# Kernel optimization log

Measured on AMD Instinct MI355X. Metric: run time of the kernel, lower is better.

The kernel has to match this reference:

```python
import jax, jax.numpy as jnp
import numpy as np

NQ = 12          # num_qubits
NL = 5           # num_layers
NA = 4           # num_actions
DIM = 2 ** NQ    # state-vector dimension

# PennyLane convention: wire 0 is the most-significant bit of the state index.
_idx = np.arange(DIM)
_bits = (_idx[:, None] >> (NQ - 1 - np.arange(NQ))) & 1           # [DIM, NQ]
_cz = np.ones(DIM)
for _i in range(NQ):                                              # ring of CZs (all diagonal -> fuse)
    _cz *= np.where((_bits[:, _i] & _bits[:, (_i + 1) % NQ]) == 1, -1.0, 1.0)
CZ_RING = jnp.asarray(_cz, dtype=jnp.complex64)                   # [DIM]
ZTAB = jnp.asarray(1 - 2 * _bits[:, :NA], dtype=jnp.float32)      # [DIM, NA] PauliZ eigenvalues


def _bc(v):
    # broadcast an angle-derived scalar or [B] vector against [B, lead, trail]
    v = jnp.asarray(v)
    return v.reshape(v.shape + (1, 1))


def _apply_1q(state, wire, m00, m01, m10, m11):
    b = state.shape[0]
    lead, trail = 2 ** wire, 2 ** (NQ - 1 - wire)
    s = state.reshape(b, lead, 2, trail)
    s0, s1 = s[:, :, 0, :], s[:, :, 1, :]
    return jnp.stack([m00 * s0 + m01 * s1, m10 * s0 + m11 * s1], axis=2).reshape(b, DIM)


def _rx(state, wire, theta):
    c = _bc(jnp.cos(0.5 * theta)).astype(jnp.complex64)
    s = _bc(jnp.sin(0.5 * theta)).astype(jnp.complex64)
    return _apply_1q(state, wire, c, -1j * s, -1j * s, c)


def _ry(state, wire, theta):
    c = _bc(jnp.cos(0.5 * theta)).astype(jnp.complex64)
    s = _bc(jnp.sin(0.5 * theta)).astype(jnp.complex64)
    return _apply_1q(state, wire, c, -s, s, c)


def _rz(state, wire, theta):
    # diagonal gate: no mixing across the wire axis
    b = state.shape[0]
    lead, trail = 2 ** wire, 2 ** (NQ - 1 - wire)
    e = _bc(jnp.exp(-0.5j * theta))  # e^{-i t/2}; conj(e) = e^{+i t/2} for real t
    s = state.reshape(b, lead, 2, trail)
    return jnp.stack([e * s[:, :, 0, :], jnp.conj(e) * s[:, :, 1, :]], axis=2).reshape(b, DIM)


def setup_inputs() -> dict:
    key = jax.random.key(0)
    k1, k2 = jax.random.split(key)
    x = jax.random.normal(k1, (4096, 4 * NQ), dtype=jnp.float32)
    input_scaling = jnp.ones((NL, 3, NQ), dtype=jnp.float32)
    weights = jax.random.uniform(k2, (NL, 3, 2 * NQ), dtype=jnp.float32,
                                 minval=-np.pi, maxval=np.pi)
    output_scaling = jnp.ones((NA,), dtype=jnp.float32)
    return {"x": x, "input_scaling": input_scaling, "weights": weights,
            "output_scaling": output_scaling}


def reference(x, input_scaling, weights, output_scaling):
    b = x.shape[0]
    feats = (x[:, NQ:2 * NQ], x[:, 2 * NQ:3 * NQ], x[:, 3 * NQ:4 * NQ])
    state = jnp.zeros((b, DIM), dtype=jnp.complex64).at[:, 0].set(1.0)
    for layer in range(NL):
        for blk in range(3):
            f = feats[blk]
            for i in range(NQ):
                state = _rx(state, i, input_scaling[layer, blk, i] * f[:, i])
            for i in range(NQ):
                state = _ry(state, i, weights[layer, blk, i])
            for i in range(NQ):
                state = _rz(state, i, weights[layer, blk, i + NQ])
            state = state * CZ_RING[None, :]
    probs = state.real ** 2 + state.imag ** 2          # [B, DIM]
    expvals = probs @ ZTAB                             # [B, NA] <Z_i>
    return expvals * output_scaling                    # logits
```

## Files before the change

kernel.cpp:

```cpp
#include <hip/hip_runtime.h>
#include <stdint.h>

#define NQ 12
#define NL 5
#define NIT 15
#define AMPS 16


typedef float f2 __attribute__((ext_vector_type(2)));

static __device__ __forceinline__ float f_u(unsigned u) { return __uint_as_float(u); }
static __device__ __forceinline__ unsigned u_f(float f) { return __float_as_uint(f); }

#define PK_MUL_RR(acc, C, S) \
    asm("v_pk_mul_f32 %0, %1, %2 op_sel_hi:[0,1]" : "=v"(acc) : "v"(C), "v"(S))
#define PK_FMA_I(acc, C, S) \
    asm("v_pk_fma_f32 %0, %1, %2, %0 op_sel:[1,1,0] op_sel_hi:[1,0,1] neg_lo:[1,0,0]" \
        : "+v"(acc) : "v"(C), "v"(S))
#define PK_FMA_R(acc, C, S) \
    asm("v_pk_fma_f32 %0, %1, %2, %0 op_sel_hi:[0,1,1]" : "+v"(acc) : "v"(C), "v"(S))
#define PK_FMA_IC(acc, C, S) \
    asm("v_pk_fma_f32 %0, %1, %2, %0 op_sel:[1,1,0] op_sel_hi:[1,0,1] neg_hi:[1,0,0]" \
        : "+v"(acc) : "v"(C), "v"(S))
#define PK_FMA_RN(acc, C, S) \
    asm("v_pk_fma_f32 %0, %1, %2, %0 op_sel_hi:[0,1,1] neg_lo:[1,0,0] neg_hi:[1,0,0]" \
        : "+v"(acc) : "v"(C), "v"(S))

#define CMUL(DST, CA, CB) \
    { PK_MUL_RR(DST, CA, CB); PK_FMA_I(DST, CA, CB); }

#define CPLX_AB(DST, CA, S, CB, O)                                    \
    { f2 t_;                                                          \
      PK_MUL_RR(t_, CA, S); PK_FMA_I(t_, CA, S);                      \
      PK_FMA_R (t_, CB, O); PK_FMA_I(t_, CB, O);                      \
      DST = t_; }

template <int CTRL>
static __device__ __forceinline__ float dpp_xor(float v) {
    int u = (int)__float_as_uint(v);
    return __uint_as_float((unsigned)__builtin_amdgcn_update_dpp(u, u, CTRL, 0xF, 0xF, false));
}
static __device__ __forceinline__ float swz_xor4(float v) {
    return f_u((unsigned)__builtin_amdgcn_ds_swizzle((int)u_f(v), 0x101F));
}

#define AB_GATE_PK(OPX)                                                 \
    _Pragma("unroll")                                                   \
    for (int r = 0; r < AMPS; ++r) {                                    \
        f2 o; o.x = OPX(s[r].x); o.y = OPX(s[r].y);                     \
        CPLX_AB(s[r], CA, s[r], CB, o)                                  \
    }

template <int ST>
static __device__ __forceinline__ void reg_gate_pk(f2 (&s)[AMPS], f2 CAg, f2 CBg) {
#pragma unroll
    for (int r0 = 0; r0 < AMPS; ++r0) {
        if (r0 & ST) continue;
        const int r1 = r0 | ST;
        const f2 s0 = s[r0], s1 = s[r1];
        f2 t0, t1;
        PK_MUL_RR(t0, CAg, s0); PK_FMA_I (t0, CAg, s0);
        PK_FMA_R (t0, CBg, s1); PK_FMA_I (t0, CBg, s1);
        PK_MUL_RR(t1, CAg, s1); PK_FMA_IC(t1, CAg, s1);
        PK_FMA_RN(t1, CBg, s0); PK_FMA_I (t1, CBg, s0);
        s[r0] = t0; s[r1] = t1;
    }
}

__global__ __launch_bounds__(256)
void qsim_kernel(
    const float* __restrict__ x,
    const float* __restrict__ iscale,
    const float* __restrict__ w,
    const float* __restrict__ oscale,
    float* __restrict__ out,
    int batch)
{
    const int tid  = threadIdx.x;
    const int lane = tid & 63;
    const int wv   = tid >> 6;
    const int b    = blockIdx.x;

    __shared__ float4 xch[8 * 256];
    __shared__ float4 coef[NIT * NQ];

    if (tid < NIT * NQ) {
        const int it  = tid / NQ;
        const int q   = tid - it * NQ;
        const int blk = it - 3 * (it / 3);
        const float* xb = x + (size_t)b * (4 * NQ);
        float f     = xb[NQ + blk * NQ + q];
        float alpha = iscale[it * NQ + q] * f;
        float beta  = w[it * 2 * NQ + q];
        float gamma = w[it * 2 * NQ + NQ + q];
        float sa, ca, sb, cb, sg, cg;
        sincosf(0.5f * alpha, &sa, &ca);
        sincosf(0.5f * beta,  &sb, &cb);
        sincosf(0.5f * gamma, &sg, &cg);
        float cbca = cb * ca, sbsa = sb * sa, sbca = sb * ca, cbsa = cb * sa;
        float ar =  cg * cbca + sg * sbsa;
        float ai =  cg * sbsa - sg * cbca;
        float br = -(cg * sbca + sg * cbsa);
        float bi =  sg * sbca - cg * cbsa;
        coef[tid] = make_float4(ar, ai, br, bi);
    }

    f2 s[AMPS];
#pragma unroll
    for (int r = 0; r < AMPS; ++r) { s[r].x = 0.f; s[r].y = 0.f; }
    if (tid == 0) s[0].x = 1.f;

    unsigned czm = 0;
#pragma unroll
    for (int r = 0; r < AMPS; ++r) {
        unsigned idx  = ((unsigned)wv << 10) | ((unsigned)lane << 4) | (unsigned)r;
        unsigned adj  = (idx & (idx >> 1)) & 0x7FFu;
        unsigned wrap = (idx & (idx >> 11)) & 1u;
        czm |= (((unsigned)__popc(adj) + wrap) & 1u) << r;
    }

    const unsigned sw1 = (unsigned)((wv >> 1) & 1) << 31;
    const unsigned sw0 = (unsigned)(wv & 1) << 31;
    const bool hb2 = (lane >> 5) & 1;
    const bool hb3 = (lane >> 4) & 1;
    const unsigned sb4 = (unsigned)((lane >> 3) & 1) << 31;
    const unsigned sb5 = (unsigned)((lane >> 2) & 1) << 31;
    const unsigned sb6 = (unsigned)((lane >> 1) & 1) << 31;
    const unsigned sb7 = (unsigned)(lane & 1) << 31;

    const int t64  = tid ^ 64;
    const int t128 = tid ^ 128;
    const int t192 = tid ^ 192;

    __syncthreads();

#pragma unroll 1
    for (int it = 0; it < NIT; ++it) {
        float4 c[NQ];
#pragma unroll
        for (int q = 0; q < NQ; ++q) c[q] = coef[it * NQ + q];

        {
            const f2 A0 = { c[0].x, f_u(u_f(c[0].y) ^ sw1) };
            const f2 B0 = { f_u(u_f(c[0].z) ^ sw1), c[0].w };
            const f2 A1 = { c[1].x, f_u(u_f(c[1].y) ^ sw0) };
            const f2 B1 = { f_u(u_f(c[1].z) ^ sw0), c[1].w };
            f2 Cs, C64, C128, C192;
            CMUL(Cs,   A0, A1)
            CMUL(C64,  A0, B1)
            CMUL(C128, B0, A1)
            CMUL(C192, B0, B1)

            __syncthreads();
#pragma unroll
            for (int k = 0; k < 8; ++k)
                xch[(k << 8) + tid] = make_float4(s[2*k].x, s[2*k].y, s[2*k+1].x, s[2*k+1].y);
            __syncthreads();
#pragma unroll
            for (int k = 0; k < 8; ++k) {
                const float4 p1 = xch[(k << 8) + t64];
                const float4 p2 = xch[(k << 8) + t128];
                const float4 p3 = xch[(k << 8) + t192];
                {
                    const f2 o1 = { p1.x, p1.y }, o2 = { p2.x, p2.y }, o3 = { p3.x, p3.y };
                    f2 t0;
                    PK_MUL_RR(t0, Cs, s[2*k]); PK_FMA_I(t0, Cs, s[2*k]);
                    PK_FMA_R(t0, C64,  o1);    PK_FMA_I(t0, C64,  o1);
                    PK_FMA_R(t0, C128, o2);    PK_FMA_I(t0, C128, o2);
                    PK_FMA_R(t0, C192, o3);    PK_FMA_I(t0, C192, o3);
                    s[2*k] = t0;
                }
                {
                    const f2 o1 = { p1.z, p1.w }, o2 = { p2.z, p2.w }, o3 = { p3.z, p3.w };
                    f2 t1;
                    PK_MUL_RR(t1, Cs, s[2*k+1]); PK_FMA_I(t1, Cs, s[2*k+1]);
                    PK_FMA_R(t1, C64,  o1);      PK_FMA_I(t1, C64,  o1);
                    PK_FMA_R(t1, C128, o2);      PK_FMA_I(t1, C128, o2);
                    PK_FMA_R(t1, C192, o3);      PK_FMA_I(t1, C192, o3);
                    s[2*k+1] = t1;
                }
            }
        }

        { const f2 CA = { c[8].x,  c[8].y  }, CB = { c[8].z,  c[8].w  }; reg_gate_pk<8>(s, CA, CB); }
        { const f2 CA = { c[9].x,  c[9].y  }, CB = { c[9].z,  c[9].w  }; reg_gate_pk<4>(s, CA, CB); }
        { const f2 CA = { c[10].x, c[10].y }, CB = { c[10].z, c[10].w }; reg_gate_pk<2>(s, CA, CB); }
        { const f2 CA = { c[11].x, c[11].y }, CB = { c[11].z, c[11].w }; reg_gate_pk<1>(s, CA, CB); }

        {
            const f2 CP = { hb2 ? -c[2].z : c[2].x, hb2 ?  c[2].w : c[2].y };
            const f2 CQ = { hb2 ?  c[2].x : c[2].z, hb2 ? -c[2].y : c[2].w };
#pragma unroll
            for (int r = 0; r < AMPS; ++r) {
                auto dx = __builtin_amdgcn_permlane32_swap(u_f(s[r].x), u_f(s[r].x), false, false);
                auto dy = __builtin_amdgcn_permlane32_swap(u_f(s[r].y), u_f(s[r].y), false, false);
                f2 na = { f_u(dx[0]), f_u(dy[0]) };
                f2 nb = { f_u(dx[1]), f_u(dy[1]) };
                CPLX_AB(s[r], CP, na, CQ, nb)
            }
        }
        {
            const f2 CP = { hb3 ? -c[3].z : c[3].x, hb3 ?  c[3].w : c[3].y };
            const f2 CQ = { hb3 ?  c[3].x : c[3].z, hb3 ? -c[3].y : c[3].w };
#pragma unroll
            for (int r = 0; r < AMPS; ++r) {
                auto dx = __builtin_amdgcn_permlane16_swap(u_f(s[r].x), u_f(s[r].x), false, false);
                auto dy = __builtin_amdgcn_permlane16_swap(u_f(s[r].y), u_f(s[r].y), false, false);
                f2 na = { f_u(dx[0]), f_u(dy[0]) };
                f2 nb = { f_u(dx[1]), f_u(dy[1]) };
                CPLX_AB(s[r], CP, na, CQ, nb)
            }
        }
        {
            const f2 CA = { c[4].x, f_u(u_f(c[4].y) ^ sb4) };
            const f2 CB = { f_u(u_f(c[4].z) ^ sb4), c[4].w };
            AB_GATE_PK(dpp_xor<0x128>)
        }
        {
            const f2 CA = { c[5].x, f_u(u_f(c[5].y) ^ sb5) };
            const f2 CB = { f_u(u_f(c[5].z) ^ sb5), c[5].w };
#pragma unroll
            for (int h = 0; h < 2; ++h) {
                float ox[8], oy[8];
#pragma unroll
                for (int r = 0; r < 8; ++r) {
                    ox[r] = swz_xor4(s[h*8 + r].x);
                    oy[r] = swz_xor4(s[h*8 + r].y);
                }
#pragma unroll
                for (int r = 0; r < 8; ++r) {
                    f2 o = { ox[r], oy[r] };
                    CPLX_AB(s[h*8 + r], CA, s[h*8 + r], CB, o)
                }
            }
        }
        {
            const f2 CA = { c[6].x, f_u(u_f(c[6].y) ^ sb6) };
            const f2 CB = { f_u(u_f(c[6].z) ^ sb6), c[6].w };
            AB_GATE_PK(dpp_xor<0x4E>)
        }
        {
            const f2 CA = { c[7].x, f_u(u_f(c[7].y) ^ sb7) };
            const f2 CB = { f_u(u_f(c[7].z) ^ sb7), c[7].w };
            AB_GATE_PK(dpp_xor<0xB1>)
        }

#pragma unroll
        for (int r = 0; r < AMPS; ++r) {
            const unsigned sgn = ((czm >> r) & 1u) << 31;
            s[r].x = f_u(u_f(s[r].x) ^ sgn);
            s[r].y = f_u(u_f(s[r].y) ^ sgn);
        }
    }

    float p = 0.f;
#pragma unroll
    for (int r = 0; r < AMPS; ++r) p = fmaf(s[r].x, s[r].x, fmaf(s[r].y, s[r].y, p));

    float v0 = ((wv   >> 1) & 1) ? -p : p;
    float v1 = ( wv         & 1) ? -p : p;
    float v2 = ((lane >> 5) & 1) ? -p : p;
    float v3 = ((lane >> 4) & 1) ? -p : p;
#pragma unroll
    for (int m = 1; m <= 32; m <<= 1) {
        v0 += __shfl_xor(v0, m);
        v1 += __shfl_xor(v1, m);
        v2 += __shfl_xor(v2, m);
        v3 += __shfl_xor(v3, m);
    }

    __syncthreads();
    if (lane == 0) xch[wv] = make_float4(v0, v1, v2, v3);
    __syncthreads();
    if (tid == 0) {
        float4 a0 = xch[0], a1 = xch[1], a2 = xch[2], a3 = xch[3];
        float4 o;
        o.x = (a0.x + a1.x + a2.x + a3.x) * oscale[0];
        o.y = (a0.y + a1.y + a2.y + a3.y) * oscale[1];
        o.z = (a0.z + a1.z + a2.z + a3.z) * oscale[2];
        o.w = (a0.w + a1.w + a2.w + a3.w) * oscale[3];
        *reinterpret_cast<float4*>(out + (size_t)b * 4) = o;
    }
}

extern "C" void kernel_launch(void* const* d_in, const int* in_sizes, int n_in,
                              void* d_out, int out_size, void* d_ws, size_t ws_size,
                              hipStream_t stream) {
    const float* x      = (const float*)d_in[0];
    const float* iscale = (const float*)d_in[1];
    const float* w      = (const float*)d_in[2];
    const float* oscale = (const float*)d_in[3];
    float* out          = (float*)d_out;

    const int batch = in_sizes[0] / (4 * NQ);
    qsim_kernel<<<batch, 256, 0, stream>>>(x, iscale, w, oscale, out, batch);
}
```

Baseline: 537.4 us.

## Replace cross-wave gate exchange with alternating qubit-layout transpose and precomputed coefficient table

The two wave-index qubits are no longer applied through an LDS exchange that reads three partner waves per amplitude. Instead, an all-to-all transpose through LDS swaps those qubits with the top two register qubits, and the qubit mapping alternates between even and odd iterations. The CZ mask and the final Z expectation reduction are adjusted to match. Coefficients are now precomputed by a separate kernel into the workspace and read from global memory, with an LDS fallback when the workspace is too small. This lowers LDS traffic per iteration, at the cost of an extra kernel launch and global coefficient loads.

```diff
diff --git a/kernel.cpp b/kernel.cpp
--- a/kernel.cpp
+++ b/kernel.cpp
@@ -5,6 +5,7 @@
 #define NL 5
 #define NIT 15
 #define AMPS 16
+#define CPB (NIT * NQ)
 
 
 typedef float f2 __attribute__((ext_vector_type(2)));
@@ -26,9 +27,6 @@
     asm("v_pk_fma_f32 %0, %1, %2, %0 op_sel_hi:[0,1,1] neg_lo:[1,0,0] neg_hi:[1,0,0]" \
         : "+v"(acc) : "v"(C), "v"(S))
 
-#define CMUL(DST, CA, CB) \
-    { PK_MUL_RR(DST, CA, CB); PK_FMA_I(DST, CA, CB); }
-
 #define CPLX_AB(DST, CA, S, CB, O)                                    \
     { f2 t_;                                                          \
       PK_MUL_RR(t_, CA, S); PK_FMA_I(t_, CA, S);                      \
@@ -67,42 +65,65 @@
     }
 }
 
-__global__ __launch_bounds__(256)
-void qsim_kernel(
+static __device__ __forceinline__ float4 build_coef(float alpha, float beta, float gamma) {
+    float sa, ca, sb, cb, sg, cg;
+    sincosf(0.5f * alpha, &sa, &ca);
+    sincosf(0.5f * beta,  &sb, &cb);
+    sincosf(0.5f * gamma, &sg, &cg);
+    float cbca = cb * ca, sbsa = sb * sa, sbca = sb * ca, cbsa = cb * sa;
+    float ar =  cg * cbca + sg * sbsa;
+    float ai =  cg * sbsa - sg * cbca;
+    float br = -(cg * sbca + sg * cbsa);
+    float bi =  sg * sbca - cg * cbsa;
+    return make_float4(ar, ai, br, bi);
+}
+
+__global__ __launch_bounds__(256) void coef_kernel(
+    const float* __restrict__ x, const float* __restrict__ iscale,
+    const float* __restrict__ w, float4* __restrict__ ctab, int total)
+{
+    int gid = blockIdx.x * 256 + threadIdx.x;
+    if (gid >= total) return;
+    int b  = gid / CPB;
+    int t  = gid - b * CPB;
+    int it = t / NQ;
+    int q  = t - it * NQ;
+    int blk = it - 3 * (it / 3);
+    float f     = x[(size_t)b * (4 * NQ) + NQ + blk * NQ + q];
+    float alpha = iscale[it * NQ + q] * f;
+    ctab[gid] = build_coef(alpha, w[it * 2 * NQ + q], w[it * 2 * NQ + NQ + q]);
+}
+
+template <bool TAB>
+__global__ __launch_bounds__(256) void qsim_kernel(
     const float* __restrict__ x,
     const float* __restrict__ iscale,
     const float* __restrict__ w,
     const float* __restrict__ oscale,
-    float* __restrict__ out,
-    int batch)
+    const float4* __restrict__ ctab,
+    float* __restrict__ out)
 {
     const int tid  = threadIdx.x;
     const int lane = tid & 63;
     const int wv   = tid >> 6;
     const int b    = blockIdx.x;
 
-    __shared__ float4 xch[8 * 256];
-    __shared__ float4 coef[NIT * NQ];
-
-    if (tid < NIT * NQ) {
-        const int it  = tid / NQ;
-        const int q   = tid - it * NQ;
-        const int blk = it - 3 * (it / 3);
-        const float* xb = x + (size_t)b * (4 * NQ);
-        float f     = xb[NQ + blk * NQ + q];
-        float alpha = iscale[it * NQ + q] * f;
-        float beta  = w[it * 2 * NQ + q];
-        float gamma = w[it * 2 * NQ + NQ + q];
-        float sa, ca, sb, cb, sg, cg;
-        sincosf(0.5f * alpha, &sa, &ca);
-        sincosf(0.5f * beta,  &sb, &cb);
-        sincosf(0.5f * gamma, &sg, &cg);
-        float cbca = cb * ca, sbsa = sb * sa, sbca = sb * ca, cbsa = cb * sa;
-        float ar =  cg * cbca + sg * sbsa;
-        float ai =  cg * sbsa - sg * cbca;
-        float br = -(cg * sbca + sg * cbsa);
-        float bi =  sg * sbca - cg * cbsa;
-        coef[tid] = make_float4(ar, ai, br, bi);
+    extern __shared__ float4 smem[];
+    float4* buf  = smem;
+    float4* clds = smem + 1536;
+
+#define TBUF(SLOT, Q) buf[((((SLOT) << 1) | (Q)) << 6) | lane]
+
+    if constexpr (!TAB) {
+        if (tid < CPB) {
+            const int it  = tid / NQ;
+            const int q   = tid - it * NQ;
+            const int blk = it - 3 * (it / 3);
+            float f     = x[(size_t)b * (4 * NQ) + NQ + blk * NQ + q];
+            float alpha = iscale[it * NQ + q] * f;
+            clds[tid] = build_coef(alpha, w[it * 2 * NQ + q], w[it * 2 * NQ + NQ + q]);
+        }
+        __syncthreads();
     }
 
     f2 s[AMPS];
@@ -110,17 +131,20 @@
     for (int r = 0; r < AMPS; ++r) { s[r].x = 0.f; s[r].y = 0.f; }
     if (tid == 0) s[0].x = 1.f;
 
-    unsigned czm = 0;
+    unsigned czmA = 0, czmB = 0;
 #pragma unroll
     for (int r = 0; r < AMPS; ++r) {
-        unsigned idx  = ((unsigned)wv << 10) | ((unsigned)lane << 4) | (unsigned)r;
-        unsigned adj  = (idx & (idx >> 1)) & 0x7FFu;
-        unsigned wrap = (idx & (idx >> 11)) & 1u;
-        czm |= (((unsigned)__popc(adj) + wrap) & 1u) << r;
-    }
-
-    const unsigned sw1 = (unsigned)((wv >> 1) & 1) << 31;
-    const unsigned sw0 = (unsigned)(wv & 1) << 31;
+        unsigned ia = ((unsigned)wv << 10) | ((unsigned)lane << 4) | (unsigned)r;
+        unsigned ib = (((unsigned)(r >> 3) & 1u) << 11) | (((unsigned)(r >> 2) & 1u) << 10)
+                    | ((unsigned)lane << 4)
+                    | (((unsigned)(wv >> 1) & 1u) << 3) | (((unsigned)wv & 1u) << 2)
+                    | ((unsigned)r & 3u);
+        unsigned pa = ((unsigned)__popc((ia & (ia >> 1)) & 0x7FFu) + ((ia & (ia >> 11)) & 1u)) & 1u;
+        unsigned pb = ((unsigned)__popc((ib & (ib >> 1)) & 0x7FFu) + ((ib & (ib >> 11)) & 1u)) & 1u;
+        czmA |= pa << r;
+        czmB |= pb << r;
+    }
+
     const bool hb2 = (lane >> 5) & 1;
     const bool hb3 = (lane >> 4) & 1;
     const unsigned sb4 = (unsigned)((lane >> 3) & 1) << 31;
@@ -128,64 +152,28 @@
     const unsigned sb6 = (unsigned)((lane >> 1) & 1) << 31;
     const unsigned sb7 = (unsigned)(lane & 1) << 31;
 
-    const int t64  = tid ^ 64;
-    const int t128 = tid ^ 128;
-    const int t192 = tid ^ 192;
-
-    __syncthreads();
+    const float4* gtab = TAB ? (ctab + (size_t)b * CPB) : nullptr;
 
 #pragma unroll 1
     for (int it = 0; it < NIT; ++it) {
         float4 c[NQ];
-#pragma unroll
-        for (int q = 0; q < NQ; ++q) c[q] = coef[it * NQ + q];
-
-        {
-            const f2 A0 = { c[0].x, f_u(u_f(c[0].y) ^ sw1) };
-            const f2 B0 = { f_u(u_f(c[0].z) ^ sw1), c[0].w };
-            const f2 A1 = { c[1].x, f_u(u_f(c[1].y) ^ sw0) };
-            const f2 B1 = { f_u(u_f(c[1].z) ^ sw0), c[1].w };
-            f2 Cs, C64, C128, C192;
-            CMUL(Cs,   A0, A1)
-            CMUL(C64,  A0, B1)
-            CMUL(C128, B0, A1)
-            CMUL(C192, B0, B1)
-
-            __syncthreads();
-#pragma unroll
-            for (int k = 0; k < 8; ++k)
-                xch[(k << 8) + tid] = make_float4(s[2*k].x, s[2*k].y, s[2*k+1].x, s[2*k+1].y);
-            __syncthreads();
-#pragma unroll
-            for (int k = 0; k < 8; ++k) {
-                const float4 p1 = xch[(k << 8) + t64];
-                const float4 p2 = xch[(k << 8) + t128];
-                const float4 p3 = xch[(k << 8) + t192];
-                {
-                    const f2 o1 = { p1.x, p1.y }, o2 = { p2.x, p2.y }, o3 = { p3.x, p3.y };
-                    f2 t0;
-                    PK_MUL_RR(t0, Cs, s[2*k]); PK_FMA_I(t0, Cs, s[2*k]);
-                    PK_FMA_R(t0, C64,  o1);    PK_FMA_I(t0, C64,  o1);
-                    PK_FMA_R(t0, C128, o2);    PK_FMA_I(t0, C128, o2);
-                    PK_FMA_R(t0, C192, o3);    PK_FMA_I(t0, C192, o3);
-                    s[2*k] = t0;
-                }
-                {
-                    const f2 o1 = { p1.z, p1.w }, o2 = { p2.z, p2.w }, o3 = { p3.z, p3.w };
-                    f2 t1;
-                    PK_MUL_RR(t1, Cs, s[2*k+1]); PK_FMA_I(t1, Cs, s[2*k+1]);
-                    PK_FMA_R(t1, C64,  o1);      PK_FMA_I(t1, C64,  o1);
-                    PK_FMA_R(t1, C128, o2);      PK_FMA_I(t1, C128, o2);
-                    PK_FMA_R(t1, C192, o3);      PK_FMA_I(t1, C192, o3);
-                    s[2*k+1] = t1;
-                }
-            }
-        }
-
-        { const f2 CA = { c[8].x,  c[8].y  }, CB = { c[8].z,  c[8].w  }; reg_gate_pk<8>(s, CA, CB); }
-        { const f2 CA = { c[9].x,  c[9].y  }, CB = { c[9].z,  c[9].w  }; reg_gate_pk<4>(s, CA, CB); }
-        { const f2 CA = { c[10].x, c[10].y }, CB = { c[10].z, c[10].w }; reg_gate_pk<2>(s, CA, CB); }
-        { const f2 CA = { c[11].x, c[11].y }, CB = { c[11].z, c[11].w }; reg_gate_pk<1>(s, CA, CB); }
+        if constexpr (TAB) {
+#pragma unroll
+            for (int q = 0; q < NQ; ++q) c[q] = gtab[it * NQ + q];
+        } else {
+#pragma unroll
+            for (int q = 0; q < NQ; ++q) c[q] = clds[it * NQ + q];
+        }
+        const bool ev = (it & 1) == 0;
+
+        {
+            const float4 c0 = ev ? c[8] : c[0];
+            const float4 c1 = ev ? c[9] : c[1];
+            { const f2 CA = { c0.x, c0.y }, CB = { c0.z, c0.w }; reg_gate_pk<8>(s, CA, CB); }
+            { const f2 CA = { c1.x, c1.y }, CB = { c1.z, c1.w }; reg_gate_pk<4>(s, CA, CB); }
+            { const f2 CA = { c[10].x, c[10].y }, CB = { c[10].z, c[10].w }; reg_gate_pk<2>(s, CA, CB); }
+            { const f2 CA = { c[11].x, c[11].y }, CB = { c[11].z, c[11].w }; reg_gate_pk<1>(s, CA, CB); }
+        }
 
         {
             const f2 CP = { hb2 ? -c[2].z : c[2].x, hb2 ?  c[2].w : c[2].y };
@@ -245,22 +233,55 @@
             AB_GATE_PK(dpp_xor<0xB1>)
         }
 
+        __syncthreads();
+#pragma unroll
+        for (int g = 0; g < 4; ++g) {
+            if (g == wv) continue;
+            const int slot = g * 3 + (wv < g ? wv : wv - 1);
+            TBUF(slot, 0) = make_float4(s[4*g+0].x, s[4*g+0].y, s[4*g+1].x, s[4*g+1].y);
+            TBUF(slot, 1) = make_float4(s[4*g+2].x, s[4*g+2].y, s[4*g+3].x, s[4*g+3].y);
+        }
+        __syncthreads();
+#pragma unroll
+        for (int h = 0; h < 4; ++h) {
+            if (h == wv) continue;
+            const int slot = wv * 3 + (h < wv ? h : h - 1);
+            const float4 pa = TBUF(slot, 0);
+            const float4 pb = TBUF(slot, 1);
+            s[4*h+0] = f2{ pa.x, pa.y }; s[4*h+1] = f2{ pa.z, pa.w };
+            s[4*h+2] = f2{ pb.x, pb.y }; s[4*h+3] = f2{ pb.z, pb.w };
+        }
+
+        {
+            const float4 c0 = ev ? c[0] : c[8];
+            const float4 c1 = ev ? c[1] : c[9];
+            { const f2 CA = { c0.x, c0.y }, CB = { c0.z, c0.w }; reg_gate_pk<8>(s, CA, CB); }
+            { const f2 CA = { c1.x, c1.y }, CB = { c1.z, c1.w }; reg_gate_pk<4>(s, CA, CB); }
+        }
+
+        const unsigned mcz = ev ? czmB : czmA;
 #pragma unroll
         for (int r = 0; r < AMPS; ++r) {
-            const unsigned sgn = ((czm >> r) & 1u) << 31;
+            const unsigned sgn = ((mcz >> r) & 1u) << 31;
             s[r].x = f_u(u_f(s[r].x) ^ sgn);
             s[r].y = f_u(u_f(s[r].y) ^ sgn);
         }
     }
 
-    float p = 0.f;
-#pragma unroll
-    for (int r = 0; r < AMPS; ++r) p = fmaf(s[r].x, s[r].x, fmaf(s[r].y, s[r].y, p));
-
-    float v0 = ((wv   >> 1) & 1) ? -p : p;
-    float v1 = ( wv         & 1) ? -p : p;
-    float v2 = ((lane >> 5) & 1) ? -p : p;
-    float v3 = ((lane >> 4) & 1) ? -p : p;
+    float pg[4];
+#pragma unroll
+    for (int g = 0; g < 4; ++g) {
+        float p = 0.f;
+#pragma unroll
+        for (int j = 0; j < 4; ++j)
+            p = fmaf(s[4*g+j].x, s[4*g+j].x, fmaf(s[4*g+j].y, s[4*g+j].y, p));
+        pg[g] = p;
+    }
+    const float ptot = (pg[0] + pg[1]) + (pg[2] + pg[3]);
+    float v0 = (pg[0] + pg[1]) - (pg[2] + pg[3]);
+    float v1 = (pg[0] + pg[2]) - (pg[1] + pg[3]);
+    float v2 = hb2 ? -ptot : ptot;
+    float v3 = hb3 ? -ptot : ptot;
 #pragma unroll
     for (int m = 1; m <= 32; m <<= 1) {
         v0 += __shfl_xor(v0, m);
@@ -270,10 +291,10 @@
     }
 
     __syncthreads();
-    if (lane == 0) xch[wv] = make_float4(v0, v1, v2, v3);
+    if (lane == 0) buf[wv] = make_float4(v0, v1, v2, v3);
     __syncthreads();
     if (tid == 0) {
-        float4 a0 = xch[0], a1 = xch[1], a2 = xch[2], a3 = xch[3];
+        float4 a0 = buf[0], a1 = buf[1], a2 = buf[2], a3 = buf[3];
         float4 o;
         o.x = (a0.x + a1.x + a2.x + a3.x) * oscale[0];
         o.y = (a0.y + a1.y + a2.y + a3.y) * oscale[1];
@@ -281,6 +302,7 @@
         o.w = (a0.w + a1.w + a2.w + a3.w) * oscale[3];
         *reinterpret_cast<float4*>(out + (size_t)b * 4) = o;
     }
+#undef TBUF
 }
 
 extern "C" void kernel_launch(void* const* d_in, const int* in_sizes, int n_in,
@@ -293,5 +315,15 @@
     float* out          = (float*)d_out;
 
     const int batch = in_sizes[0] / (4 * NQ);
-    qsim_kernel<<<batch, 256, 0, stream>>>(x, iscale, w, oscale, out, batch);
-}
+    const size_t need = (size_t)batch * CPB * sizeof(float4);
+
+    if (ws_size >= need) {
+        const int total = batch * CPB;
+        coef_kernel<<<(total + 255) / 256, 256, 0, stream>>>(x, iscale, w, (float4*)d_ws, total);
+        qsim_kernel<true><<<batch, 256, 12 * 2 * 64 * sizeof(float4), stream>>>(
+            x, iscale, w, oscale, (const float4*)d_ws, out);
+    } else {
+        qsim_kernel<false><<<batch, 256, (12 * 2 * 64 + CPB) * sizeof(float4), stream>>>(
+            x, iscale, w, oscale, nullptr, out);
+    }
+}
```

After: 568.8 us. 5.8% more time.
